# Performance work log

Hardware: AMD Instinct MI355X
Metric: run time of the kernel (lower is better)

The kernel has to match this reference:

```python
import jax, jax.numpy as jnp
import numpy as np

N, C, A, H, O, T = 18, 4, 14, 20, 8, 5  # nodes, classes, alarms, hidden, out, time steps


def _lin(key, dout, din, std):
    W = std * jax.random.normal(key, (dout, din), jnp.float32)
    b = jnp.zeros((dout,), jnp.float32)
    return W, b


def setup_inputs():
    key = jax.random.key(0)
    ks = jax.random.split(key, 12)
    adj = (jax.random.uniform(ks[0], (N, N)) < 0.3).astype(jnp.float32)  # binary adjacency
    x = jax.random.normal(ks[1], (N, H), jnp.float32)
    Wz, bz = _lin(ks[2], H, 2 * H, 0.1)
    Uz, buz = _lin(ks[3], H, H, 0.1)
    Wr, br = _lin(ks[4], H, 2 * H, 0.1)
    Ur, bur = _lin(ks[5], H, H, 0.1)
    Ww, bw = _lin(ks[6], H, 2 * H, 0.1)
    Uw, bu = _lin(ks[7], H, H, 0.1)
    Wo, bo = _lin(ks[8], O, 2 * H, 0.1)
    Wx, bx = _lin(ks[9], O, H, 0.01)
    Wy, by = _lin(ks[10], O, H, 0.01)
    w2, b2 = _lin(ks[11], 1, O, 0.1)
    return {"x": x, "adj": adj, "Wz": Wz, "bz": bz, "Uz": Uz, "buz": buz,
            "Wr": Wr, "br": br, "Ur": Ur, "bur": bur, "Ww": Ww, "bw": bw,
            "Uw": Uw, "bu": bu, "Wo": Wo, "bo": bo, "Wx": Wx, "bx": bx,
            "Wy": Wy, "by": by, "w2": w2, "b2": b2}


def reference(x, adj, Wz, bz, Uz, buz, Wr, br, Ur, bur, Ww, bw, Uw, bu,
              Wo, bo, Wx, bx, Wy, by, w2, b2):
    in_mat, out_mat = adj, adj.T  # split_matrix: in=A, out=A^T

    def step(h, _):
        # message aggregation over in/out edges, then GRU gates (eqs 3-5)
        a = jnp.concatenate([in_mat @ h, out_mat @ h], axis=1)        # [N, 2H]
        z = jax.nn.sigmoid(a @ Wz.T + bz + h @ Uz.T + buz)            # update gate
        r = jax.nn.sigmoid(a @ Wr.T + br + h @ Ur.T + bur)            # reset gate
        hg = jnp.tanh(a @ Ww.T + bw + (r * h) @ Uw.T + bu)            # candidate
        return (1.0 - z) * h + z * hg, None

    h, _ = jax.lax.scan(step, x, None, length=T)                       # [N, H]
    out = jnp.tanh(jnp.concatenate([h, x], axis=1) @ Wo.T + bo)        # [N, O]

    # attention-style reasoning between class nodes and alarm nodes
    cfcx = jnp.tanh(h[:C] @ Wx.T + bx)                                 # [C, O]
    afcy = jnp.tanh(h[C:] @ Wy.T + by)                                 # [A, O]
    cacat = cfcx[:, None, :] * afcy[None, :, :]                        # [C, A, O]
    rfc = jax.nn.sigmoid(jnp.einsum('cao,o->ca', cacat, w2[0]) + b2[0])[..., None]
    mask = in_mat[:C, C:][..., None]                                   # [C, A, 1]
    rfc = rfc * mask

    weighted = out[C:][None, :, :] * rfc                               # [C, A, O]
    final = jnp.concatenate([out[:C][:, None, :], weighted], axis=1)   # [C, 1+A, O]
    return final
```

## Files before the change

kernel.cpp:

```cpp
#include <hip/hip_runtime.h>


#define NN 18
#define CC 4
#define AA_ 14
#define HH 20
#define OO 8
#define TT 5

__global__ __launch_bounds__(512, 1) void ggnn_fused(
    const float* __restrict__ x,  const float* __restrict__ adj,
    const float* __restrict__ Wz, const float* __restrict__ bz,
    const float* __restrict__ Uz, const float* __restrict__ buz,
    const float* __restrict__ Wr, const float* __restrict__ br,
    const float* __restrict__ Ur, const float* __restrict__ bur,
    const float* __restrict__ Ww, const float* __restrict__ bw,
    const float* __restrict__ Uw, const float* __restrict__ bu,
    const float* __restrict__ Wo, const float* __restrict__ bo,
    const float* __restrict__ Wx, const float* __restrict__ bx,
    const float* __restrict__ Wy, const float* __restrict__ by,
    const float* __restrict__ w2, const float* __restrict__ b2,
    float* __restrict__ outp)
{
    __shared__ float sWz[HH*2*HH], sWr[HH*2*HH], sWw[HH*2*HH];
    __shared__ float sUz[HH*HH], sUr[HH*HH], sUw[HH*HH];
    __shared__ float sbz[HH], sbuz[HH], sbr[HH], sbur[HH], sbw[HH], sbu[HH];
    __shared__ float sWo[OO*2*HH], sbo[OO], sWx[OO*HH], sbx[OO], sWy[OO*HH], sby[OO];
    __shared__ float sw2[OO], sb2;
    __shared__ float sAdj[NN*NN], sX[NN*HH];
    __shared__ float h[NN*HH], aa[NN*2*HH], rr[NN*HH], zz[NN*HH], ws[NN*HH];
    __shared__ float sOut[NN*OO], sCf[CC*OO], sAf[AA_*OO], sRfc[CC*AA_];

    const int tid = threadIdx.x;

    for (int i = tid; i < HH*2*HH; i += 512) { sWz[i]=Wz[i]; sWr[i]=Wr[i]; sWw[i]=Ww[i]; }
    for (int i = tid; i < HH*HH;  i += 512) { sUz[i]=Uz[i]; sUr[i]=Ur[i]; sUw[i]=Uw[i]; }
    if (tid < HH) { sbz[tid]=bz[tid]; sbuz[tid]=buz[tid]; sbr[tid]=br[tid];
                    sbur[tid]=bur[tid]; sbw[tid]=bw[tid]; sbu[tid]=bu[tid]; }
    for (int i = tid; i < OO*2*HH; i += 512) sWo[i]=Wo[i];
    for (int i = tid; i < OO*HH;  i += 512) { sWx[i]=Wx[i]; sWy[i]=Wy[i]; }
    if (tid < OO) { sbo[tid]=bo[tid]; sbx[tid]=bx[tid]; sby[tid]=by[tid]; sw2[tid]=w2[tid]; }
    if (tid == 0) sb2 = b2[0];
    for (int i = tid; i < NN*NN; i += 512) sAdj[i]=adj[i];
    for (int i = tid; i < NN*HH; i += 512) { float v = x[i]; sX[i]=v; h[i]=v; }
    __syncthreads();

    for (int t = 0; t < TT; ++t) {
        for (int i = tid; i < NN*2*HH; i += 512) {
            int n = i / (2*HH), k = i % (2*HH);
            float s = 0.f;
            if (k < HH) {
                #pragma unroll
                for (int m = 0; m < NN; ++m) s += sAdj[n*NN+m]*h[m*HH+k];
            } else {
                int kk = k - HH;
                #pragma unroll
                for (int m = 0; m < NN; ++m) s += sAdj[m*NN+n]*h[m*HH+kk];
            }
            aa[i] = s;
        }
        __syncthreads();
        if (tid < NN*HH) {
            int n = tid / HH, i = tid % HH;
            float sz = sbz[i] + sbuz[i];
            float sr = sbr[i] + sbur[i];
            float sw_ = sbw[i];
            #pragma unroll
            for (int k = 0; k < 2*HH; ++k) {
                float av = aa[n*2*HH+k];
                sz += sWz[i*2*HH+k]*av;
                sr += sWr[i*2*HH+k]*av;
                sw_ += sWw[i*2*HH+k]*av;
            }
            #pragma unroll
            for (int j = 0; j < HH; ++j) {
                float hv = h[n*HH+j];
                sz += sUz[i*HH+j]*hv;
                sr += sUr[i*HH+j]*hv;
            }
            zz[tid] = 1.f/(1.f+expf(-sz));
            rr[tid] = 1.f/(1.f+expf(-sr));
            ws[tid] = sw_;
        }
        __syncthreads();
        float hnew = 0.f;
        if (tid < NN*HH) {
            int n = tid / HH, i = tid % HH;
            float s = ws[tid] + sbu[i];
            #pragma unroll
            for (int j = 0; j < HH; ++j) s += sUw[i*HH+j]*rr[n*HH+j]*h[n*HH+j];
            float hg = tanhf(s);
            float zv = zz[tid];
            hnew = (1.f - zv)*h[tid] + zv*hg;
        }
        __syncthreads();
        if (tid < NN*HH) h[tid] = hnew;
        __syncthreads();
    }

    if (tid < NN*OO) {
        int n = tid / OO, o = tid % OO;
        float s = sbo[o];
        #pragma unroll
        for (int j = 0; j < HH; ++j) s += sWo[o*2*HH+j]*h[n*HH+j];
        #pragma unroll
        for (int j = 0; j < HH; ++j) s += sWo[o*2*HH+HH+j]*sX[n*HH+j];
        sOut[tid] = tanhf(s);
    } else if (tid >= 256 && tid < 256 + CC*OO) {
        int i = tid - 256;
        int c = i / OO, o = i % OO;
        float s = sbx[o];
        #pragma unroll
        for (int j = 0; j < HH; ++j) s += sWx[o*HH+j]*h[c*HH+j];
        sCf[i] = tanhf(s);
    } else if (tid >= 320 && tid < 320 + AA_*OO) {
        int i = tid - 320;
        int a = i / OO, o = i % OO;
        float s = sby[o];
        #pragma unroll
        for (int j = 0; j < HH; ++j) s += sWy[o*HH+j]*h[(CC+a)*HH+j];
        sAf[i] = tanhf(s);
    }
    __syncthreads();

    if (tid < CC*AA_) {
        int c = tid / AA_, a = tid % AA_;
        float s = sb2;
        #pragma unroll
        for (int o = 0; o < OO; ++o) s += sCf[c*OO+o]*sAf[a*OO+o]*sw2[o];
        sRfc[tid] = (1.f/(1.f+expf(-s))) * sAdj[c*NN + CC + a];
    }
    __syncthreads();

    if (tid < CC*(1+AA_)*OO) {
        int c = tid / ((1+AA_)*OO);
        int rem = tid % ((1+AA_)*OO);
        int s_ = rem / OO, o = rem % OO;
        float v;
        if (s_ == 0) v = sOut[c*OO+o];
        else         v = sOut[(CC + s_-1)*OO + o] * sRfc[c*AA_ + (s_-1)];
        outp[tid] = v;
    }
}

extern "C" void kernel_launch(void* const* d_in, const int* in_sizes, int n_in,
                              void* d_out, int out_size, void* d_ws, size_t ws_size,
                              hipStream_t stream) {
    (void)in_sizes; (void)n_in; (void)d_ws; (void)ws_size; (void)out_size;
    const float* x   = (const float*)d_in[0];
    const float* adj = (const float*)d_in[1];
    const float* Wz  = (const float*)d_in[2];
    const float* bz  = (const float*)d_in[3];
    const float* Uz  = (const float*)d_in[4];
    const float* buz = (const float*)d_in[5];
    const float* Wr  = (const float*)d_in[6];
    const float* br  = (const float*)d_in[7];
    const float* Ur  = (const float*)d_in[8];
    const float* bur = (const float*)d_in[9];
    const float* Ww  = (const float*)d_in[10];
    const float* bw  = (const float*)d_in[11];
    const float* Uw  = (const float*)d_in[12];
    const float* bu  = (const float*)d_in[13];
    const float* Wo  = (const float*)d_in[14];
    const float* bo  = (const float*)d_in[15];
    const float* Wx  = (const float*)d_in[16];
    const float* bx  = (const float*)d_in[17];
    const float* Wy  = (const float*)d_in[18];
    const float* by  = (const float*)d_in[19];
    const float* w2  = (const float*)d_in[20];
    const float* b2  = (const float*)d_in[21];
    float* outp = (float*)d_out;

    ggnn_fused<<<1, 512, 0, stream>>>(x, adj, Wz, bz, Uz, buz, Wr, br, Ur, bur,
                                      Ww, bw, Uw, bu, Wo, bo, Wx, bx, Wy, by,
                                      w2, b2, outp);
}
```

Measured before the change: 23.24 us.

## Keep GRU weights in registers, transpose hidden state, split gates across waves

Rewrites the fused GGNN kernel so each thread holds its row of the gate weights in float4 registers instead of copying every weight matrix into shared memory. Hidden state and aggregated messages are stored transposed, with node as the fastest index, to spread shared-memory accesses across banks. The z and r gates are computed by separate wave groups on 768 threads, and the hidden state is double-buffered to remove one barrier per step. Fast __expf-based sigmoid and tanh replace expf/tanhf, which trades some accuracy for cheaper math, and register pressure rises.

```diff
diff --git a/kernel.cpp b/kernel.cpp
--- a/kernel.cpp
+++ b/kernel.cpp
@@ -1,14 +1,10 @@
 #include <hip/hip_runtime.h>
 
 
-#define NN 18
-#define CC 4
-#define AA_ 14
-#define HH 20
-#define OO 8
-#define TT 5
-
-__global__ __launch_bounds__(512, 1) void ggnn_fused(
+__device__ __forceinline__ float fsig(float x){ return 1.0f/(1.0f+__expf(-x)); }
+__device__ __forceinline__ float ftnh(float x){ return 1.0f - 2.0f/(__expf(2.0f*x)+1.0f); }
+
+__global__ __launch_bounds__(768, 1) void ggnn_fused(
     const float* __restrict__ x,  const float* __restrict__ adj,
     const float* __restrict__ Wz, const float* __restrict__ bz,
     const float* __restrict__ Uz, const float* __restrict__ buz,
@@ -22,156 +18,203 @@
     const float* __restrict__ w2, const float* __restrict__ b2,
     float* __restrict__ outp)
 {
-    __shared__ float sWz[HH*2*HH], sWr[HH*2*HH], sWw[HH*2*HH];
-    __shared__ float sUz[HH*HH], sUr[HH*HH], sUw[HH*HH];
-    __shared__ float sbz[HH], sbuz[HH], sbr[HH], sbur[HH], sbw[HH], sbu[HH];
-    __shared__ float sWo[OO*2*HH], sbo[OO], sWx[OO*HH], sbx[OO], sWy[OO*HH], sby[OO];
-    __shared__ float sw2[OO], sb2;
-    __shared__ float sAdj[NN*NN], sX[NN*HH];
-    __shared__ float h[NN*HH], aa[NN*2*HH], rr[NN*HH], zz[NN*HH], ws[NN*HH];
-    __shared__ float sOut[NN*OO], sCf[CC*OO], sAf[AA_*OO], sRfc[CC*AA_];
-
-    const int tid = threadIdx.x;
-
-    for (int i = tid; i < HH*2*HH; i += 512) { sWz[i]=Wz[i]; sWr[i]=Wr[i]; sWw[i]=Ww[i]; }
-    for (int i = tid; i < HH*HH;  i += 512) { sUz[i]=Uz[i]; sUr[i]=Ur[i]; sUw[i]=Uw[i]; }
-    if (tid < HH) { sbz[tid]=bz[tid]; sbuz[tid]=buz[tid]; sbr[tid]=br[tid];
-                    sbur[tid]=bur[tid]; sbw[tid]=bw[tid]; sbu[tid]=bu[tid]; }
-    for (int i = tid; i < OO*2*HH; i += 512) sWo[i]=Wo[i];
-    for (int i = tid; i < OO*HH;  i += 512) { sWx[i]=Wx[i]; sWy[i]=Wy[i]; }
-    if (tid < OO) { sbo[tid]=bo[tid]; sbx[tid]=bx[tid]; sby[tid]=by[tid]; sw2[tid]=w2[tid]; }
-    if (tid == 0) sb2 = b2[0];
-    for (int i = tid; i < NN*NN; i += 512) sAdj[i]=adj[i];
-    for (int i = tid; i < NN*HH; i += 512) { float v = x[i]; sX[i]=v; h[i]=v; }
+  __shared__ float sAdj[324];
+  __shared__ float hA[360], hB[360];
+  __shared__ float aaT[720];
+  __shared__ float rrT[360], ws1[360];
+  __shared__ float sOut[144], sCf[32], sAf[112], sRfc[56];
+
+  const int tid = threadIdx.x;
+
+  const int g    = (tid >> 6) & 1;
+  const int idx  = (tid >> 7) * 64 + (tid & 63);
+  const bool act2 = (idx < 360);
+  const int i2 = idx / 18, n2 = idx % 18;
+
+  const bool act1 = (tid < 720);
+  const int n1 = tid % 18;
+  const int kk = tid / 18;
+  const int k1 = kk % 20;
+  const int abase = (kk < 20) ? (n1 * 18) : n1;
+  const int astep = (kk < 20) ? 1 : 18;
+
+  if (tid < 324) sAdj[tid] = adj[tid];
+  if (tid < 360) { int j = tid/18, n = tid%18; hA[j*18+n] = x[n*20+j]; }
+
+  float4 w4[10], u4[5], wh4[5], uw4[5];
+  float bias1 = 0.f, bwi = 0.f, bui = 0.f;
+  if (act2) {
+    const float* Wg = g ? Wr : Wz;
+    const float* Ug = g ? Ur : Uz;
+    #pragma unroll
+    for (int q=0;q<10;q++) w4[q] = *(const float4*)(Wg + i2*40 + 4*q);
+    #pragma unroll
+    for (int q=0;q<5;q++){
+      u4[q]  = *(const float4*)(Ug + i2*20 + 4*q);
+      wh4[q] = *(const float4*)(Ww + i2*40 + g*20 + 4*q);
+    }
+    if (g == 0){
+      bias1 = bz[i2] + buz[i2];
+      bwi   = bw[i2];
+      bui   = bu[i2];
+      #pragma unroll
+      for (int q=0;q<5;q++) uw4[q] = *(const float4*)(Uw + i2*20 + 4*q);
+    } else {
+      bias1 = br[i2] + bur[i2];
+    }
+  }
+  __syncthreads();
+
+  float* hc = hA;
+  float* hn = hB;
+  float zreg = 0.f, sw0 = 0.f;
+
+  for (int t=0;t<5;t++){
+    if (act1){
+      float s = 0.f;
+      #pragma unroll
+      for (int m=0;m<18;m++) s += sAdj[abase + m*astep] * hc[k1*18+m];
+      aaT[kk*18 + n1] = s;
+    }
     __syncthreads();
 
-    for (int t = 0; t < TT; ++t) {
-        for (int i = tid; i < NN*2*HH; i += 512) {
-            int n = i / (2*HH), k = i % (2*HH);
-            float s = 0.f;
-            if (k < HH) {
-                #pragma unroll
-                for (int m = 0; m < NN; ++m) s += sAdj[n*NN+m]*h[m*HH+k];
-            } else {
-                int kk = k - HH;
-                #pragma unroll
-                for (int m = 0; m < NN; ++m) s += sAdj[m*NN+n]*h[m*HH+kk];
-            }
-            aa[i] = s;
-        }
-        __syncthreads();
-        if (tid < NN*HH) {
-            int n = tid / HH, i = tid % HH;
-            float sz = sbz[i] + sbuz[i];
-            float sr = sbr[i] + sbur[i];
-            float sw_ = sbw[i];
-            #pragma unroll
-            for (int k = 0; k < 2*HH; ++k) {
-                float av = aa[n*2*HH+k];
-                sz += sWz[i*2*HH+k]*av;
-                sr += sWr[i*2*HH+k]*av;
-                sw_ += sWw[i*2*HH+k]*av;
-            }
-            #pragma unroll
-            for (int j = 0; j < HH; ++j) {
-                float hv = h[n*HH+j];
-                sz += sUz[i*HH+j]*hv;
-                sr += sUr[i*HH+j]*hv;
-            }
-            zz[tid] = 1.f/(1.f+expf(-sz));
-            rr[tid] = 1.f/(1.f+expf(-sr));
-            ws[tid] = sw_;
-        }
-        __syncthreads();
-        float hnew = 0.f;
-        if (tid < NN*HH) {
-            int n = tid / HH, i = tid % HH;
-            float s = ws[tid] + sbu[i];
-            #pragma unroll
-            for (int j = 0; j < HH; ++j) s += sUw[i*HH+j]*rr[n*HH+j]*h[n*HH+j];
-            float hg = tanhf(s);
-            float zv = zz[tid];
-            hnew = (1.f - zv)*h[tid] + zv*hg;
-        }
-        __syncthreads();
-        if (tid < NN*HH) h[tid] = hnew;
-        __syncthreads();
-    }
-
-    if (tid < NN*OO) {
-        int n = tid / OO, o = tid % OO;
-        float s = sbo[o];
-        #pragma unroll
-        for (int j = 0; j < HH; ++j) s += sWo[o*2*HH+j]*h[n*HH+j];
-        #pragma unroll
-        for (int j = 0; j < HH; ++j) s += sWo[o*2*HH+HH+j]*sX[n*HH+j];
-        sOut[tid] = tanhf(s);
-    } else if (tid >= 256 && tid < 256 + CC*OO) {
-        int i = tid - 256;
-        int c = i / OO, o = i % OO;
-        float s = sbx[o];
-        #pragma unroll
-        for (int j = 0; j < HH; ++j) s += sWx[o*HH+j]*h[c*HH+j];
-        sCf[i] = tanhf(s);
-    } else if (tid >= 320 && tid < 320 + AA_*OO) {
-        int i = tid - 320;
-        int a = i / OO, o = i % OO;
-        float s = sby[o];
-        #pragma unroll
-        for (int j = 0; j < HH; ++j) s += sWy[o*HH+j]*h[(CC+a)*HH+j];
-        sAf[i] = tanhf(s);
+    if (act2){
+      float sg = bias1, sw = bwi;
+      #pragma unroll
+      for (int q=0;q<10;q++){
+        float a0 = aaT[(4*q+0)*18+n2];
+        float a1 = aaT[(4*q+1)*18+n2];
+        float a2 = aaT[(4*q+2)*18+n2];
+        float a3 = aaT[(4*q+3)*18+n2];
+        sg += w4[q].x*a0 + w4[q].y*a1 + w4[q].z*a2 + w4[q].w*a3;
+        if (g==0 && q<5)  { sw += wh4[q].x*a0 + wh4[q].y*a1 + wh4[q].z*a2 + wh4[q].w*a3; }
+        if (g==1 && q>=5) { const float4 W = wh4[q-5]; sw += W.x*a0 + W.y*a1 + W.z*a2 + W.w*a3; }
+      }
+      #pragma unroll
+      for (int q=0;q<5;q++){
+        float h0 = hc[(4*q+0)*18+n2];
+        float h1 = hc[(4*q+1)*18+n2];
+        float h2 = hc[(4*q+2)*18+n2];
+        float h3 = hc[(4*q+3)*18+n2];
+        sg += u4[q].x*h0 + u4[q].y*h1 + u4[q].z*h2 + u4[q].w*h3;
+      }
+      if (g == 0){
+        zreg = fsig(sg);
+        sw0  = sw;
+      } else {
+        rrT[i2*18+n2] = fsig(sg);
+        ws1[i2*18+n2] = sw;
+      }
     }
     __syncthreads();
 
-    if (tid < CC*AA_) {
-        int c = tid / AA_, a = tid % AA_;
-        float s = sb2;
-        #pragma unroll
-        for (int o = 0; o < OO; ++o) s += sCf[c*OO+o]*sAf[a*OO+o]*sw2[o];
-        sRfc[tid] = (1.f/(1.f+expf(-s))) * sAdj[c*NN + CC + a];
+    if (g == 0 && act2){
+      float s = bui + sw0 + ws1[i2*18+n2];
+      #pragma unroll
+      for (int q=0;q<5;q++){
+        float u0=u4[0].x;
+        (void)u0;
+        s += uw4[q].x * rrT[(4*q+0)*18+n2] * hc[(4*q+0)*18+n2];
+        s += uw4[q].y * rrT[(4*q+1)*18+n2] * hc[(4*q+1)*18+n2];
+        s += uw4[q].z * rrT[(4*q+2)*18+n2] * hc[(4*q+2)*18+n2];
+        s += uw4[q].w * rrT[(4*q+3)*18+n2] * hc[(4*q+3)*18+n2];
+      }
+      float hg = ftnh(s);
+      hn[i2*18+n2] = (1.f - zreg)*hc[i2*18+n2] + zreg*hg;
     }
     __syncthreads();
-
-    if (tid < CC*(1+AA_)*OO) {
-        int c = tid / ((1+AA_)*OO);
-        int rem = tid % ((1+AA_)*OO);
-        int s_ = rem / OO, o = rem % OO;
-        float v;
-        if (s_ == 0) v = sOut[c*OO+o];
-        else         v = sOut[(CC + s_-1)*OO + o] * sRfc[c*AA_ + (s_-1)];
-        outp[tid] = v;
-    }
+    float* tmp = hc; hc = hn; hn = tmp;
+  }
+
+  if (tid < 144){
+    int n_ = tid/8, o = tid%8;
+    float s = bo[o];
+    #pragma unroll
+    for (int q=0;q<5;q++){
+      float4 w = *(const float4*)(Wo + o*40 + 4*q);
+      s += w.x*hc[(4*q+0)*18+n_] + w.y*hc[(4*q+1)*18+n_]
+         + w.z*hc[(4*q+2)*18+n_] + w.w*hc[(4*q+3)*18+n_];
+    }
+    #pragma unroll
+    for (int q=0;q<5;q++){
+      float4 w  = *(const float4*)(Wo + o*40 + 20 + 4*q);
+      float4 xv = *(const float4*)(x + n_*20 + 4*q);
+      s += w.x*xv.x + w.y*xv.y + w.z*xv.z + w.w*xv.w;
+    }
+    sOut[tid] = ftnh(s);
+  } else if (tid >= 192 && tid < 224){
+    int ii = tid-192; int c = ii/8, o = ii%8;
+    float s = bx[o];
+    #pragma unroll
+    for (int q=0;q<5;q++){
+      float4 w = *(const float4*)(Wx + o*20 + 4*q);
+      s += w.x*hc[(4*q+0)*18+c] + w.y*hc[(4*q+1)*18+c]
+         + w.z*hc[(4*q+2)*18+c] + w.w*hc[(4*q+3)*18+c];
+    }
+    sCf[ii] = ftnh(s);
+  } else if (tid >= 256 && tid < 368){
+    int ii = tid-256; int a = ii/8, o = ii%8;
+    float s = by[o];
+    #pragma unroll
+    for (int q=0;q<5;q++){
+      float4 w = *(const float4*)(Wy + o*20 + 4*q);
+      s += w.x*hc[(4*q+0)*18+4+a] + w.y*hc[(4*q+1)*18+4+a]
+         + w.z*hc[(4*q+2)*18+4+a] + w.w*hc[(4*q+3)*18+4+a];
+    }
+    sAf[ii] = ftnh(s);
+  }
+  __syncthreads();
+
+  if (tid < 56){
+    int c = tid/14, a = tid%14;
+    float4 w20 = *(const float4*)(w2);
+    float4 w21 = *(const float4*)(w2+4);
+    const float* cf = &sCf[c*8];
+    const float* af = &sAf[a*8];
+    float s = b2[0];
+    s += cf[0]*af[0]*w20.x + cf[1]*af[1]*w20.y + cf[2]*af[2]*w20.z + cf[3]*af[3]*w20.w;
+    s += cf[4]*af[4]*w21.x + cf[5]*af[5]*w21.y + cf[6]*af[6]*w21.z + cf[7]*af[7]*w21.w;
+    sRfc[tid] = fsig(s) * sAdj[c*18 + 4 + a];
+  }
+  __syncthreads();
+
+  if (tid < 480){
+    int c = tid/120, rem = tid%120, s_ = rem/8, o = rem%8;
+    float v = (s_ == 0) ? sOut[c*8+o]
+                        : sOut[(3+s_)*8+o] * sRfc[c*14 + (s_-1)];
+    outp[tid] = v;
+  }
 }
 
 extern "C" void kernel_launch(void* const* d_in, const int* in_sizes, int n_in,
                               void* d_out, int out_size, void* d_ws, size_t ws_size,
                               hipStream_t stream) {
-    (void)in_sizes; (void)n_in; (void)d_ws; (void)ws_size; (void)out_size;
-    const float* x   = (const float*)d_in[0];
-    const float* adj = (const float*)d_in[1];
-    const float* Wz  = (const float*)d_in[2];
-    const float* bz  = (const float*)d_in[3];
-    const float* Uz  = (const float*)d_in[4];
-    const float* buz = (const float*)d_in[5];
-    const float* Wr  = (const float*)d_in[6];
-    const float* br  = (const float*)d_in[7];
-    const float* Ur  = (const float*)d_in[8];
-    const float* bur = (const float*)d_in[9];
-    const float* Ww  = (const float*)d_in[10];
-    const float* bw  = (const float*)d_in[11];
-    const float* Uw  = (const float*)d_in[12];
-    const float* bu  = (const float*)d_in[13];
-    const float* Wo  = (const float*)d_in[14];
-    const float* bo  = (const float*)d_in[15];
-    const float* Wx  = (const float*)d_in[16];
-    const float* bx  = (const float*)d_in[17];
-    const float* Wy  = (const float*)d_in[18];
-    const float* by  = (const float*)d_in[19];
-    const float* w2  = (const float*)d_in[20];
-    const float* b2  = (const float*)d_in[21];
-    float* outp = (float*)d_out;
-
-    ggnn_fused<<<1, 512, 0, stream>>>(x, adj, Wz, bz, Uz, buz, Wr, br, Ur, bur,
-                                      Ww, bw, Uw, bu, Wo, bo, Wx, bx, Wy, by,
-                                      w2, b2, outp);
+  (void)in_sizes; (void)n_in; (void)d_ws; (void)ws_size; (void)out_size;
+  const float* x   = (const float*)d_in[0];
+  const float* adj = (const float*)d_in[1];
+  const float* Wz  = (const float*)d_in[2];
+  const float* bz  = (const float*)d_in[3];
+  const float* Uz  = (const float*)d_in[4];
+  const float* buz = (const float*)d_in[5];
+  const float* Wr  = (const float*)d_in[6];
+  const float* br  = (const float*)d_in[7];
+  const float* Ur  = (const float*)d_in[8];
+  const float* bur = (const float*)d_in[9];
+  const float* Ww  = (const float*)d_in[10];
+  const float* bw  = (const float*)d_in[11];
+  const float* Uw  = (const float*)d_in[12];
+  const float* bu  = (const float*)d_in[13];
+  const float* Wo  = (const float*)d_in[14];
+  const float* bo  = (const float*)d_in[15];
+  const float* Wx  = (const float*)d_in[16];
+  const float* bx  = (const float*)d_in[17];
+  const float* Wy  = (const float*)d_in[18];
+  const float* by  = (const float*)d_in[19];
+  const float* w2  = (const float*)d_in[20];
+  const float* b2  = (const float*)d_in[21];
+  float* outp = (float*)d_out;
+
+  ggnn_fused<<<1, 768, 0, stream>>>(x, adj, Wz, bz, Uz, buz, Wr, br, Ur, bur,
+                                    Ww, bw, Uw, bu, Wo, bo, Wx, bx, Wy, by,
+                                    w2, b2, outp);
 }
```

Measured after the change: 20.22 us. 13.0% less time.
